# Kernel optimization log

Hardware: AMD Instinct MI355X
Metric: run time of the kernel (lower is better)

Reference implementation:

```python
import jax, jax.numpy as jnp
import numpy as np
from jax import lax

GAMMA = 1.0
BIG = 1e10  # finite 'infinity' to keep softmin gradients well-defined
EPS = 1e-8


def _cosine_cost(x, y):
    # x: [B,M,D], y: [B,N,D] -> cost [B,M,N] = 1 - cos_sim
    xn = x / (jnp.linalg.norm(x, axis=-1, keepdims=True) + EPS)
    yn = y / (jnp.linalg.norm(y, axis=-1, keepdims=True) + EPS)
    return 1.0 - jnp.einsum('bmd,bnd->bmn', xn, yn)


def _softdtw_from_cost(D, gamma=GAMMA):
    # Anti-diagonal soft-DTW DP. D: [B,M,N] -> [B]
    B, M, N = D.shape
    ii = jnp.arange(M + 1)
    prev = jnp.full((B, M + 1), BIG, D.dtype).at[:, 0].set(0.0)  # diag k=0
    prev2 = jnp.full((B, M + 1), BIG, D.dtype)                   # diag k=-1

    def shift(a):  # a[i] -> a[i-1], pad with BIG
        return jnp.concatenate([jnp.full((B, 1), BIG, a.dtype), a[:, :-1]], axis=1)

    def step(carry, k):
        p2, p1 = carry
        jj = k - ii
        valid = (ii >= 1) & (jj >= 1) & (ii <= M) & (jj <= N)
        di = jnp.clip(ii - 1, 0, M - 1)
        dj = jnp.clip(jj - 1, 0, N - 1)
        d = D[:, di, dj]                      # [B, M+1] cost along diagonal
        a = shift(p1)                          # R[i-1, j]
        b = p1                                 # R[i, j-1]
        c = shift(p2)                          # R[i-1, j-1]
        smin = -gamma * jax.nn.logsumexp(jnp.stack([-a, -b, -c]) / gamma, axis=0)
        new = jnp.where(valid[None, :], d + smin, BIG)
        return (p1, new), None

    (_, last), _ = lax.scan(step, (prev2, prev), jnp.arange(1, M + N + 1))
    return last[:, M]  # R[M, N]


def _sdtw(x, y):
    # SoftDTW(gamma=1, normalize=True, dist='cosine')
    raw_xy = _softdtw_from_cost(_cosine_cost(x, y))
    raw_xx = _softdtw_from_cost(_cosine_cost(x, x))
    raw_yy = _softdtw_from_cost(_cosine_cost(y, y))
    return raw_xy - 0.5 * (raw_xx + raw_yy)


def setup_inputs() -> dict:
    key = jax.random.key(0)
    k1, k2, k3, k4 = jax.random.split(key, 4)
    B, T, D = 32, 512, 128
    return {
        'TGT': jax.random.normal(k1, (B, T, D), jnp.float32),
        'OTH': jax.random.normal(k2, (B, T, D), jnp.float32),
        'X': jax.random.normal(k3, (B, T, D), jnp.float32),
        'labels': jax.random.normal(k4, (B,), jnp.float32),
    }


def reference(TGT, OTH, X, labels):
    diff = _sdtw(OTH, X) - _sdtw(TGT, X)   # [B]
    return jnp.mean((diff - labels) ** 2)  # MSELoss
```

## Files before the change

kernel.cpp:

```cpp
#include <hip/hip_runtime.h>
#include <hip/hip_bf16.h>

#define LOG2E 1.4426950408889634f
#define LN2   0.6931471805599453f
#define BIGP  (1.0e10f * LOG2E)

#define BATCH 32
#define SEQ   512
#define DIM   128
#define NMAT  128

#define EXP2F(x) __builtin_amdgcn_exp2f(x)
#define LOG2F(x) __builtin_amdgcn_logf(x)

typedef short bf16x8 __attribute__((ext_vector_type(8)));
typedef float f32x4 __attribute__((ext_vector_type(4)));
typedef __attribute__((address_space(1))) const void gas_void;
typedef __attribute__((address_space(3))) void las_void;

__device__ __forceinline__ float dpp_shr1(float x) {
  return __int_as_float(__builtin_amdgcn_update_dpp(
      0, __float_as_int(x), 0x138, 0xF, 0xF, false));
}
__device__ __forceinline__ float dpp_shl1(float x) {
  return __int_as_float(__builtin_amdgcn_update_dpp(
      0, __float_as_int(x), 0x130, 0xF, 0xF, false));
}

__device__ __forceinline__ unsigned short f2bf_rn(float f) {
  unsigned u = __float_as_uint(f);
  u = (u + 0x7FFF + ((u >> 16) & 1)) >> 16;
  return (unsigned short)u;
}
__device__ __forceinline__ float bf2f(unsigned short h) {
  return __uint_as_float(((unsigned)h) << 16);
}

__global__ __launch_bounds__(256) void prep_kernel(
    const float* __restrict__ tgt, const float* __restrict__ oth,
    const float* __restrict__ x, unsigned short* __restrict__ Y) {
  int gid  = blockIdx.x * blockDim.x + threadIdx.x;
  int wave = gid >> 6;
  int lane = threadIdx.x & 63;
  int set = wave / (BATCH * SEQ);
  int row = wave % (BATCH * SEQ);
  const float* src = (set == 0) ? tgt : ((set == 1) ? oth : x);
  const float2* p = (const float2*)(src + (size_t)row * DIM);
  float2 v = p[lane];
  float s = v.x * v.x + v.y * v.y;
#pragma unroll
  for (int off = 32; off; off >>= 1) s += __shfl_xor(s, off);
  float inv = 1.0f / (sqrtf(s) + 1e-8f);
  float y0 = v.x * inv, y1 = v.y * inv;
  unsigned short h0 = f2bf_rn(y0);
  unsigned short l0 = f2bf_rn(y0 - bf2f(h0));
  unsigned short h1 = f2bf_rn(y1);
  unsigned short l1 = f2bf_rn(y1 - bf2f(h1));
  ushort4 st = {h0, l0, h1, l1};
  ((ushort4*)(Y + (size_t)wave * 256))[lane] = st;
}

__global__ __launch_bounds__(256) void costmm_kernel(
    const unsigned short* __restrict__ Y, float* __restrict__ Dband) {
  __shared__ unsigned short As[64 * 64];
  __shared__ unsigned short Bs[192 * 64];

  const int s = blockIdx.x;
  const int m = blockIdx.y;
  const int p = m >> 5, b = m & 31;
  const int setA = (p == 1 || p == 3) ? 0 : 1;
  const int setB = (p <= 1) ? 2 : setA;
  const unsigned short* YA = Y + ((size_t)(setA * BATCH + b)) * SEQ * 256;
  const unsigned short* YB = Y + ((size_t)(setB * BATCH + b)) * SEQ * 256;
  const int i0 = s * 64;
  const int j0 = s * 64 - 64;

  const int t = threadIdx.x;
  const int w = t >> 6, l = t & 63;

  f32x4 acc[4][3];
#pragma unroll
  for (int a = 0; a < 4; ++a)
#pragma unroll
    for (int c = 0; c < 3; ++c) acc[a][c] = (f32x4){0.f, 0.f, 0.f, 0.f};

  const int srow_off = l >> 3;
  const int scb      = ((l & 7) * 16) ^ ((srow_off & 7) * 16);

  for (int slab = 0; slab < 4; ++slab) {
    if (slab) __syncthreads();
#pragma unroll
    for (int q2 = 0; q2 < 2; ++q2) {
      int wi = w * 2 + q2;
      int r = wi * 8 + srow_off;
      const unsigned short* gA = YA + (size_t)(i0 + r) * 256 + slab * 64 + (scb >> 1);
      __builtin_amdgcn_global_load_lds((gas_void*)gA, (las_void*)(As + wi * 512), 16, 0, 0);
    }
#pragma unroll
    for (int q6 = 0; q6 < 6; ++q6) {
      int wi = w * 6 + q6;
      int r = wi * 8 + srow_off;
      int j = j0 + r; j = (j < 0) ? 0 : ((j > 511) ? 511 : j);
      const unsigned short* gB = YB + (size_t)j * 256 + slab * 64 + (scb >> 1);
      __builtin_amdgcn_global_load_lds((gas_void*)gB, (las_void*)(Bs + wi * 512), 16, 0, 0);
    }
    asm volatile("s_waitcnt vmcnt(0)" ::: "memory");
    __syncthreads();

#pragma unroll
    for (int ks = 0; ks < 2; ++ks) {
      bf16x8 af[4], bfr[3];
#pragma unroll
      for (int f = 0; f < 4; ++f) {
        int ra = f * 16 + (l & 15);
        int ca = (ks * 64 + (l >> 4) * 16) ^ ((ra & 7) << 4);
        af[f] = *(const bf16x8*)((const char*)As + ra * 128 + ca);
      }
#pragma unroll
      for (int f = 0; f < 3; ++f) {
        int rb = w * 48 + f * 16 + (l & 15);
        int cb = (ks * 64 + (l >> 4) * 16) ^ ((rb & 7) << 4);
        bfr[f] = *(const bf16x8*)((const char*)Bs + rb * 128 + cb);
      }
#pragma unroll
      for (int fm = 0; fm < 4; ++fm)
#pragma unroll
        for (int fn = 0; fn < 3; ++fn)
          acc[fm][fn] = __builtin_amdgcn_mfma_f32_16x16x32_bf16(
              af[fm], bfr[fn], acc[fm][fn], 0, 0, 0);
    }
  }

  float* Dbm = Dband + (size_t)m * (SEQ * 128);
#pragma unroll
  for (int fm = 0; fm < 4; ++fm)
#pragma unroll
    for (int fn = 0; fn < 3; ++fn)
#pragma unroll
      for (int q = 0; q < 4; ++q) {
        int r = fm * 16 + (l >> 4) * 4 + q;
        int c = w * 48 + fn * 16 + (l & 15);
        unsigned crm = (unsigned)(c - r);
        if (crm < 128u)
          Dbm[((size_t)(i0 + r) << 7) + crm] = (1.0f - acc[fm][fn][q]) * LOG2E;
      }
}

__global__ __launch_bounds__(64) void dtw_kernel(
    const float* __restrict__ Dband, float* __restrict__ raw) {
  __shared__ float stg[128][128];
  const int t = threadIdx.x;
  const int m = blockIdx.x;
  const float* Db = Dband + (size_t)m * (SEQ * 128);

  const int d0 = 2 * t - 64, d1 = d0 + 1;
  const int ad0 = (d0 < 0) ? -d0 : d0;
  const int ad1 = (d1 < 0) ? -d1 : d1;
  const int lo0 = 2 + ad0, span0 = 1022 - 2 * ad0;
  const int lo1 = 2 + ad1, span1 = 1022 - 2 * ad1;

  float v0 = (t == 32) ? 1.0f : 0.0f;
  float v1 = 0.0f;
  int otally = 0;

#pragma unroll
  for (int q = 0; q < 32; ++q) {
    int row = q * 2;
    __builtin_amdgcn_global_load_lds(
        (gas_void*)(Db + (size_t)row * 128 + t * 4),
        (las_void*)(&stg[row][0]), 16, 0, 0);
  }

  for (int c = 0; c < 32; ++c) {
    {
      int rbase = 16 * c + 64;
#pragma unroll
      for (int q = 0; q < 8; ++q) {
        int row = rbase + q * 2;
        int srow = row + (t >> 5);
        srow = (srow > 511) ? 511 : srow;
        __builtin_amdgcn_global_load_lds(
            (gas_void*)(Db + (size_t)srow * 128 + (t & 31) * 4),
            (las_void*)(&stg[row & 127][0]), 16, 0, 0);
      }
    }
    asm volatile("s_waitcnt vmcnt(8)" ::: "memory");

    float sv[32];
    const int Lb = 32 * c + 1;
#pragma unroll
    for (int q = 0; q < 32; ++q) {
      int L = Lb + q;
      int col = 2 * t + (L & 1);
      int row = (L - col + 62) >> 1;
      float d = stg[row & 127][col];
      float e2 = EXP2F(-d);
      unsigned rel = (unsigned)(L - ((q & 1) ? lo0 : lo1));
      unsigned spn = (unsigned)((q & 1) ? span0 : span1);
      sv[q] = (rel <= spn) ? e2 : 0.0f;
    }

#pragma unroll
    for (int qq = 0; qq < 32; qq += 2) {
      {
        float a = dpp_shl1(v0);
        v1 = sv[qq] * (a + v0 + v1);
      }
      {
        float bb = dpp_shr1(v1);
        v0 = sv[qq + 1] * (v1 + bb + v0);
      }
    }

    float mx = fmaxf(v0, v1);
#pragma unroll
    for (int off = 32; off; off >>= 1) mx = fmaxf(mx, __shfl_xor(mx, off));
    int e = (int)((__float_as_uint(mx) >> 23) & 255u) - 127;
    float scale = __uint_as_float((unsigned)(127 - e) << 23);
    v0 *= scale; v1 *= scale;
    otally += e;
  }

  if (t == 32) raw[m] = -(LOG2F(v0) + (float)otally) * LN2;
}

__global__ __launch_bounds__(64) void combine_kernel(
    const float* __restrict__ raw, const float* __restrict__ labels,
    float* __restrict__ out) {
  int lane = threadIdx.x;
  float val = 0.0f;
  if (lane < BATCH) {
    float r0 = raw[0 * BATCH + lane];
    float r1 = raw[1 * BATCH + lane];
    float r2 = raw[2 * BATCH + lane];
    float r3 = raw[3 * BATCH + lane];
    float diff = r0 - r1 - 0.5f * r2 + 0.5f * r3;
    float e = diff - labels[lane];
    val = e * e;
  }
#pragma unroll
  for (int off = 32; off; off >>= 1) val += __shfl_xor(val, off);
  if (lane == 0) out[0] = val * (1.0f / BATCH);
}

extern "C" void kernel_launch(void* const* d_in, const int* in_sizes, int n_in,
                              void* d_out, int out_size, void* d_ws, size_t ws_size,
                              hipStream_t stream) {
  const float* TGT = (const float*)d_in[0];
  const float* OTH = (const float*)d_in[1];
  const float* X   = (const float*)d_in[2];
  const float* labels = (const float*)d_in[3];
  float* out = (float*)d_out;

  char* ws = (char*)d_ws;
  float* Dband = (float*)ws;
  size_t dband_bytes = (size_t)NMAT * SEQ * 128 * 4;
  unsigned short* Y = (unsigned short*)(ws + dband_bytes);
  float* raw = (float*)(ws + dband_bytes + (size_t)3 * BATCH * SEQ * 256 * 2);

  hipLaunchKernelGGL(prep_kernel, dim3((3 * BATCH * SEQ) / 4), dim3(256), 0, stream,
                     TGT, OTH, X, Y);
  hipLaunchKernelGGL(costmm_kernel, dim3(8, NMAT), dim3(256), 0, stream, Y, Dband);
  hipLaunchKernelGGL(dtw_kernel, dim3(NMAT), dim3(64), 0, stream, Dband, raw);
  hipLaunchKernelGGL(combine_kernel, dim3(1), dim3(64), 0, stream, raw, labels, out);
}
```

Measured before the change: 69.40 us.

## Precompute exp2 and validity mask in costmm; vectorize DTW loads; DPP max reduction

The cost kernel now stores exp2(-d) directly, with out-of-range columns zeroed, so the serial DTW kernel no longer computes exponentials or per-element band masks. DTW diagonal reads become paired float2 LDS loads with a simple row-range check. The per-chunk wave max reduction switches from shfl_xor to DPP row ops plus readlane to shorten the latency-bound serial path. The zeroing of invalid cells relies on the band/row masking now matching the previous lo/span logic.

```diff
diff --git a/kernel.cpp b/kernel.cpp
--- a/kernel.cpp
+++ b/kernel.cpp
@@ -25,6 +25,12 @@
 __device__ __forceinline__ float dpp_shl1(float x) {
   return __int_as_float(__builtin_amdgcn_update_dpp(
       0, __float_as_int(x), 0x130, 0xF, 0xF, false));
+}
+template <int CTRL>
+__device__ __forceinline__ float dpp_max(float x) {
+  int y = __builtin_amdgcn_update_dpp(
+      __float_as_int(x), __float_as_int(x), CTRL, 0xF, 0xF, false);
+  return fmaxf(x, __int_as_float(y));
 }
 
 __device__ __forceinline__ unsigned short f2bf_rn(float f) {
@@ -61,7 +67,7 @@
 }
 
 __global__ __launch_bounds__(256) void costmm_kernel(
-    const unsigned short* __restrict__ Y, float* __restrict__ Dband) {
+    const unsigned short* __restrict__ Y, float* __restrict__ Sband) {
   __shared__ unsigned short As[64 * 64];
   __shared__ unsigned short Bs[192 * 64];
 
@@ -131,7 +137,7 @@
     }
   }
 
-  float* Dbm = Dband + (size_t)m * (SEQ * 128);
+  float* Sbm = Sband + (size_t)m * (SEQ * 128);
 #pragma unroll
   for (int fm = 0; fm < 4; ++fm)
 #pragma unroll
@@ -141,23 +147,21 @@
         int r = fm * 16 + (l >> 4) * 4 + q;
         int c = w * 48 + fn * 16 + (l & 15);
         unsigned crm = (unsigned)(c - r);
-        if (crm < 128u)
-          Dbm[((size_t)(i0 + r) << 7) + crm] = (1.0f - acc[fm][fn][q]) * LOG2E;
+        if (crm < 128u) {
+          int jreal = j0 + c;
+          float dp = (1.0f - acc[fm][fn][q]) * LOG2E;
+          float sval = ((unsigned)jreal < 512u) ? EXP2F(-dp) : 0.0f;
+          Sbm[((size_t)(i0 + r) << 7) + crm] = sval;
+        }
       }
 }
 
 __global__ __launch_bounds__(64) void dtw_kernel(
-    const float* __restrict__ Dband, float* __restrict__ raw) {
+    const float* __restrict__ Sband, float* __restrict__ raw) {
   __shared__ float stg[128][128];
   const int t = threadIdx.x;
   const int m = blockIdx.x;
-  const float* Db = Dband + (size_t)m * (SEQ * 128);
-
-  const int d0 = 2 * t - 64, d1 = d0 + 1;
-  const int ad0 = (d0 < 0) ? -d0 : d0;
-  const int ad1 = (d1 < 0) ? -d1 : d1;
-  const int lo0 = 2 + ad0, span0 = 1022 - 2 * ad0;
-  const int lo1 = 2 + ad1, span1 = 1022 - 2 * ad1;
+  const float* Db = Sband + (size_t)m * (SEQ * 128);
 
   float v0 = (t == 32) ? 1.0f : 0.0f;
   float v1 = 0.0f;
@@ -188,16 +192,23 @@
 
     float sv[32];
     const int Lb = 32 * c + 1;
-#pragma unroll
-    for (int q = 0; q < 32; ++q) {
-      int L = Lb + q;
-      int col = 2 * t + (L & 1);
-      int row = (L - col + 62) >> 1;
-      float d = stg[row & 127][col];
-      float e2 = EXP2F(-d);
-      unsigned rel = (unsigned)(L - ((q & 1) ? lo0 : lo1));
-      unsigned spn = (unsigned)((q & 1) ? span0 : span1);
-      sv[q] = (rel <= spn) ? e2 : 0.0f;
+    const int ra = ((Lb + 61) >> 1) - t;
+    {
+      float xx = stg[ra & 127][2 * t + 1];
+      sv[0] = ((unsigned)ra < 512u) ? xx : 0.0f;
+    }
+#pragma unroll
+    for (int k = 1; k <= 15; ++k) {
+      int row = ra + k;
+      float2 xy = *(const float2*)&stg[row & 127][2 * t];
+      bool ok = (unsigned)row < 512u;
+      sv[2 * k - 1] = ok ? xy.x : 0.0f;
+      sv[2 * k]     = ok ? xy.y : 0.0f;
+    }
+    {
+      int row = ra + 16;
+      float xx = stg[row & 127][2 * t];
+      sv[31] = ((unsigned)row < 512u) ? xx : 0.0f;
     }
 
 #pragma unroll
@@ -213,9 +224,15 @@
     }
 
     float mx = fmaxf(v0, v1);
-#pragma unroll
-    for (int off = 32; off; off >>= 1) mx = fmaxf(mx, __shfl_xor(mx, off));
-    int e = (int)((__float_as_uint(mx) >> 23) & 255u) - 127;
+    mx = dpp_max<0x111>(mx);
+    mx = dpp_max<0x112>(mx);
+    mx = dpp_max<0x114>(mx);
+    mx = dpp_max<0x118>(mx);
+    mx = dpp_max<0x142>(mx);
+    mx = dpp_max<0x143>(mx);
+    float mxs = __int_as_float(
+        __builtin_amdgcn_readlane(__float_as_int(mx), 63));
+    int e = (int)((__float_as_uint(mxs) >> 23) & 255u) - 127;
     float scale = __uint_as_float((unsigned)(127 - e) << 23);
     v0 *= scale; v1 *= scale;
     otally += e;
@@ -253,14 +270,14 @@
   float* out = (float*)d_out;
 
   char* ws = (char*)d_ws;
-  float* Dband = (float*)ws;
-  size_t dband_bytes = (size_t)NMAT * SEQ * 128 * 4;
-  unsigned short* Y = (unsigned short*)(ws + dband_bytes);
-  float* raw = (float*)(ws + dband_bytes + (size_t)3 * BATCH * SEQ * 256 * 2);
+  float* Sband = (float*)ws;
+  size_t sband_bytes = (size_t)NMAT * SEQ * 128 * 4;
+  unsigned short* Y = (unsigned short*)(ws + sband_bytes);
+  float* raw = (float*)(ws + sband_bytes + (size_t)3 * BATCH * SEQ * 256 * 2);
 
   hipLaunchKernelGGL(prep_kernel, dim3((3 * BATCH * SEQ) / 4), dim3(256), 0, stream,
                      TGT, OTH, X, Y);
-  hipLaunchKernelGGL(costmm_kernel, dim3(8, NMAT), dim3(256), 0, stream, Y, Dband);
-  hipLaunchKernelGGL(dtw_kernel, dim3(NMAT), dim3(64), 0, stream, Dband, raw);
+  hipLaunchKernelGGL(costmm_kernel, dim3(8, NMAT), dim3(256), 0, stream, Y, Sband);
+  hipLaunchKernelGGL(dtw_kernel, dim3(NMAT), dim3(64), 0, stream, Sband, raw);
   hipLaunchKernelGGL(combine_kernel, dim3(1), dim3(64), 0, stream, raw, labels, out);
 }
```

New measurement: 69.06 us. About the same (-0.5%).
